# Optimization experiments

Hardware: AMD Instinct MI355X
Metric: run time of the kernel (lower is better)

## Reference

```python
import jax, jax.numpy as jnp
import numpy as np

NUM_AGENTS = 256
STATE_DIM = 12 * NUM_AGENTS
CONTROL_DIM = 4 * NUM_AGENTS
MASS = 0.5
HIDDEN = 100
BATCH = 8192


def lambertw(x):
    # Principal branch for x >= 0 via Halley iterations (jit/vjp friendly).
    w = jnp.log1p(x)
    for _ in range(30):
        ew = jnp.exp(w)
        f = w * ew - x
        denom = ew * (w + 1.0) - (w + 2.0) * f / (2.0 * (w + 1.0))
        w = w - f / denom
    return w


def setup_inputs() -> dict:
    key = jax.random.key(0)
    ks = jax.random.split(key, 8)
    scale1 = 1.0 / np.sqrt(STATE_DIM + 1)
    scale2 = 1.0 / np.sqrt(HIDDEN)
    return {
        "z": jax.random.normal(ks[0], (BATCH, STATE_DIM), dtype=jnp.float32),
        "t": jax.random.uniform(ks[1], (BATCH, 1), dtype=jnp.float32),
        "W1": jax.random.normal(ks[2], (STATE_DIM + 1, HIDDEN), dtype=jnp.float32) * scale1,
        "b1": jnp.zeros((HIDDEN,), dtype=jnp.float32),
        "W2": jax.random.normal(ks[3], (HIDDEN, HIDDEN), dtype=jnp.float32) * scale2,
        "b2": jnp.zeros((HIDDEN,), dtype=jnp.float32),
        "W3": jax.random.normal(ks[4], (HIDDEN, STATE_DIM), dtype=jnp.float32) * scale2,
        "b3": jnp.zeros((STATE_DIM,), dtype=jnp.float32),
    }


def reference(z, t, W1, b1, W2, b2, W3, b3):
    # p_net: MLP on (t, z) producing cost parameters p (B, STATE_DIM)
    x = jnp.concatenate([t, z], axis=-1)
    h = jnp.tanh(x @ W1 + b1)
    h = jnp.tanh(h @ W2 + b2)
    p = h @ W3 + b3

    B = p.shape[0]
    pr = p.reshape(B, NUM_AGENTS, 12)
    # Linear cost vector c over controls: agent components (x,y,z adjoints)/m, psi, theta, phi.
    c = jnp.stack(
        [(pr[..., 6] + pr[..., 7] + pr[..., 8]) / MASS, pr[..., 9], pr[..., 10], pr[..., 11]],
        axis=-1,
    ).reshape(B, CONTROL_DIM)

    # Closed-form solution of min_u c^T u + exp(alpha * ||u||^2), alpha = 0.5/N:
    # u* = -k c with 2*alpha*k*exp(alpha*k^2*s) = 1, s = ||c||^2
    # => k = sqrt(W(s/(2*alpha)) / (2*alpha*s))
    alpha = 0.5 / NUM_AGENTS
    s = jnp.sum(c * c, axis=-1)  # (B,)
    w = lambertw(s / (2.0 * alpha))
    safe_s = jnp.where(s > 0, s, 1.0)
    k = jnp.sqrt(w / (2.0 * alpha * safe_s))
    k = jnp.where(s > 0, k, 0.0)
    ustar = -k[:, None] * c  # (B, CONTROL_DIM)
    return ustar
```

## Files before the change

### kernel.cpp

```cpp
#include <hip/hip_runtime.h>

#define DEV __device__ __forceinline__

typedef __bf16 bf16x8 __attribute__((ext_vector_type(8)));
typedef float f32x4 __attribute__((ext_vector_type(4)));
typedef short s16x8 __attribute__((ext_vector_type(8)));
typedef unsigned short u16x8 __attribute__((ext_vector_type(8)));

constexpr int B_ = 8192;
constexpr int S_ = 3072;
constexpr int H_ = 100;
constexpr int NP_ = 128;
constexpr int C_ = 1024;
constexpr int KS_ = 64;
constexpr int NSPLIT_ = 8;
constexpr int KSP_ = S_ / NSPLIT_;
constexpr int NIT_ = KSP_ / KS_;
constexpr int MT_ = 64;

constexpr size_t OFF_W1b = 0;
constexpr size_t OFF_W2b = OFF_W1b + (size_t)NP_ * S_ * 2;
constexpr size_t OFF_W3c = OFF_W2b + (size_t)NP_ * NP_ * 2;
constexpr size_t OFF_b3c = OFF_W3c + (size_t)C_ * NP_ * 2;
constexpr size_t OFF_part = OFF_b3c + (size_t)C_ * 4;

DEV unsigned short f2bf(float f) {
  union { float f; unsigned u; } x; x.f = f;
  return (unsigned short)((x.u + 0x7FFFu + ((x.u >> 16) & 1u)) >> 16);
}

DEV float lambertw0(float x) {
  float w = log1pf(x);
#pragma unroll
  for (int i = 0; i < 10; ++i) {
    float ew = expf(w);
    float f = fmaf(w, ew, -x);
    float wp1 = w + 1.0f;
    float den = ew * wp1 - (w + 2.0f) * f / (2.0f * wp1);
    w = w - f / den;
  }
  return w;
}

DEV void gload16(const void* g, void* l) {
  __builtin_amdgcn_global_load_lds((const __attribute__((address_space(1))) unsigned int*)g,
                                   (__attribute__((address_space(3))) unsigned int*)l, 16, 0, 0);
}

__global__ void k0_prep(const float* __restrict__ W1, const float* __restrict__ W2,
                        const float* __restrict__ W3, const float* __restrict__ b3,
                        unsigned char* __restrict__ ws) {
  int idx = blockIdx.x * 256 + threadIdx.x;
  constexpr int R1 = NP_ * S_;
  constexpr int R2 = R1 + NP_ * NP_;
  constexpr int R3 = R2 + C_ * NP_;
  constexpr int R4 = R3 + C_;
  if (idx < R1) {
    int n = idx / S_, k = idx - n * S_;
    float v = (n < H_) ? W1[(size_t)(k + 1) * H_ + n] : 0.0f;
    ((unsigned short*)(ws + OFF_W1b))[idx] = f2bf(v);
  } else if (idx < R2) {
    int j = idx - R1;
    int n = j >> 7, k = j & 127;
    float v = (n < H_ && k < H_) ? W2[(size_t)k * H_ + n] : 0.0f;
    ((unsigned short*)(ws + OFF_W2b))[j] = f2bf(v);
  } else if (idx < R3) {
    int j = idx - R2;
    int n = j >> 7, k = j & 127;
    float v = 0.0f;
    if (k < H_) {
      int a = n >> 2, cmp = n & 3;
      const float* row = W3 + (size_t)k * S_ + a * 12;
      v = (cmp == 0) ? 2.0f * (row[6] + row[7] + row[8]) : row[8 + cmp];
    }
    ((unsigned short*)(ws + OFF_W3c))[j] = f2bf(v);
  } else if (idx < R4) {
    int n = idx - R3;
    int a = n >> 2, cmp = n & 3;
    const float* row = b3 + a * 12;
    float v = (cmp == 0) ? 2.0f * (row[6] + row[7] + row[8]) : row[8 + cmp];
    ((float*)(ws + OFF_b3c))[n] = v;
  }
}

__global__ __launch_bounds__(256, 4) void k1_gemm1(
    const float* __restrict__ z, const unsigned char* __restrict__ wsr,
    float* __restrict__ part) {
  __shared__ __align__(16) unsigned char ldsB[2][16384];

  const int tid = threadIdx.x;
  const int lane = tid & 63;
  const int w = tid >> 6;
  const int bid = blockIdx.x;
  const int rt = bid >> 3;
  const int h = bid & 7;
  const int rowbase = rt * MT_;
  const int k0 = h * KSP_;

  const unsigned short* W1b = (const unsigned short*)(wsr + OFF_W1b);

  const int arow = rowbase + w * 16 + (lane & 15);
  const int o8 = (lane >> 4) * 8;
  const float* zrp = z + (size_t)arow * S_ + k0 + o8;

  const int w4 = w * 4;
  const unsigned short* bsrc = W1b + (size_t)(w4 * 8 + (lane >> 3)) * S_ + k0
                               + (((lane & 7) ^ (lane >> 3)) * 8);

  const int kb0 = (lane >> 4) * 16;

  f32x4 acc[8];
#pragma unroll
  for (int e = 0; e < 8; ++e) acc[e] = f32x4{0.f, 0.f, 0.f, 0.f};

#define GLOAD_B(buf, kof) do {                                               \
    _Pragma("unroll")                                                        \
    for (int s = 0; s < 4; ++s)                                              \
      gload16(bsrc + (size_t)s * 8 * S_ + (kof),                             \
              ldsB[buf] + (w4 + s) * 1024);                                  \
  } while (0)

#define ISSUE_A(F0A, F0B, F1A, F1B, kof) do {                                \
    (F0A) = *(const float4*)(zrp + (kof));                                   \
    (F0B) = *(const float4*)(zrp + (kof) + 4);                               \
    (F1A) = *(const float4*)(zrp + (kof) + 32);                              \
    (F1B) = *(const float4*)(zrp + (kof) + 36);                              \
  } while (0)

#define COMPUTE(F0A, F0B, F1A, F1B, buf) do {                                \
    union { u16x8 u; bf16x8 b; } a0c, a1c;                                   \
    a0c.u[0] = f2bf((F0A).x); a0c.u[1] = f2bf((F0A).y);                      \
    a0c.u[2] = f2bf((F0A).z); a0c.u[3] = f2bf((F0A).w);                      \
    a0c.u[4] = f2bf((F0B).x); a0c.u[5] = f2bf((F0B).y);                      \
    a0c.u[6] = f2bf((F0B).z); a0c.u[7] = f2bf((F0B).w);                      \
    a1c.u[0] = f2bf((F1A).x); a1c.u[1] = f2bf((F1A).y);                      \
    a1c.u[2] = f2bf((F1A).z); a1c.u[3] = f2bf((F1A).w);                      \
    a1c.u[4] = f2bf((F1B).x); a1c.u[5] = f2bf((F1B).y);                      \
    a1c.u[6] = f2bf((F1B).z); a1c.u[7] = f2bf((F1B).w);                      \
    _Pragma("unroll")                                                        \
    for (int e = 0; e < 8; ++e) {                                            \
      int n = e * 16 + (lane & 15);                                          \
      bf16x8 bb0 = *(const bf16x8*)(ldsB[buf] + ((n * 128 + 0 + kb0) ^ ((n & 7) << 4)));  \
      bf16x8 bb1 = *(const bf16x8*)(ldsB[buf] + ((n * 128 + 64 + kb0) ^ ((n & 7) << 4))); \
      acc[e] = __builtin_amdgcn_mfma_f32_16x16x32_bf16(a0c.b, bb0, acc[e], 0, 0, 0);      \
      acc[e] = __builtin_amdgcn_mfma_f32_16x16x32_bf16(a1c.b, bb1, acc[e], 0, 0, 0);      \
    }                                                                        \
  } while (0)

  float4 e0a, e0b, e1a, e1b;
  float4 o0a, o0b, o1a, o1b;

  GLOAD_B(0, 0);
  ISSUE_A(e0a, e0b, e1a, e1b, 0);
  __syncthreads();

  for (int tt = 0; tt < NIT_; tt += 2) {
    {
      const bool more = (tt + 1 < NIT_);
      if (more) {
        GLOAD_B(1, (size_t)(tt + 1) * KS_);
        ISSUE_A(o0a, o0b, o1a, o1b, (tt + 1) * KS_);
      }
      COMPUTE(e0a, e0b, e1a, e1b, 0);
      __syncthreads();
    }
    {
      const bool more = (tt + 2 < NIT_);
      if (more) {
        GLOAD_B(0, (size_t)(tt + 2) * KS_);
        ISSUE_A(e0a, e0b, e1a, e1b, (tt + 2) * KS_);
      }
      COMPUTE(o0a, o0b, o1a, o1b, 1);
      __syncthreads();
    }
  }
#undef GLOAD_B
#undef ISSUE_A
#undef COMPUTE

  float* pout = part + (size_t)h * B_ * NP_;
#pragma unroll
  for (int e = 0; e < 8; ++e) {
    int col = e * 16 + (lane & 15);
#pragma unroll
    for (int i = 0; i < 4; ++i) {
      int r = w * 16 + ((lane >> 4) << 2) + i;
      pout[(size_t)(rowbase + r) * NP_ + col] = acc[e][i];
    }
  }
}

__global__ __launch_bounds__(512, 2) void k2_fused(
    const float* __restrict__ part, const float* __restrict__ t,
    const float* __restrict__ W1, const float* __restrict__ b1,
    const float* __restrict__ b2, const unsigned char* __restrict__ wsr,
    float* __restrict__ uo) {
  __shared__ __align__(16) unsigned char ldsA[8192];
  __shared__ __align__(16) unsigned char ldsB[2][32768];
  __shared__ float s_part[32][4];
  __shared__ float k_lds[32];

  const int tid = threadIdx.x;
  const int lane = tid & 63;
  const int w = tid >> 6;
  const int m = w & 1;
  const int q = w >> 1;
  const int rowbase = blockIdx.x * 32;

  const unsigned short* W2b = (const unsigned short*)(wsr + OFF_W2b);
  const unsigned short* W3cb = (const unsigned short*)(wsr + OFF_W3c);
  const float* b3c = (const float*)(wsr + OFF_b3c);

  {
    const int row = tid >> 4;
    const int col0 = (tid & 15) * 8;
    const float* p0 = part + (size_t)(rowbase + row) * NP_ + col0;
    f32x4 v[2];
#pragma unroll
    for (int p = 0; p < 2; ++p) {
      v[p] = *(const f32x4*)(p0 + p * 4);
#pragma unroll
      for (int hh = 1; hh < NSPLIT_; ++hh) {
        f32x4 u2 = *(const f32x4*)(p0 + (size_t)hh * B_ * NP_ + p * 4);
        v[p][0] += u2[0]; v[p][1] += u2[1]; v[p][2] += u2[2]; v[p][3] += u2[3];
      }
    }
    const float tv = t[rowbase + row];
    u16x8 o;
#pragma unroll
    for (int j = 0; j < 8; ++j) {
      int col = col0 + j;
      float b1c = (col < H_) ? b1[col] : 0.0f;
      float w1t = (col < H_) ? W1[col] : 0.0f;
      float pre = v[j >> 2][j & 3] + b1c + tv * w1t;
      o[j] = f2bf(tanhf(pre));
    }
    *(u16x8*)(ldsA + ((row * 256 + col0 * 2) ^ ((row & 7) << 4))) = o;
  }
#pragma unroll
  for (int s = 0; s < 4; ++s) {
    int p = s * 512 + tid;
    int n = p >> 4, k16 = p & 15;
    s16x8 v2 = *(const s16x8*)(W2b + n * 128 + k16 * 8);
    *(s16x8*)(ldsB[1] + ((n * 256 + k16 * 16) ^ ((n & 7) << 4))) = v2;
    s16x8 v3 = *(const s16x8*)(W3cb + (size_t)n * NP_ + k16 * 8);
    *(s16x8*)(ldsB[0] + ((n * 256 + k16 * 16) ^ ((n & 7) << 4))) = v3;
  }
  if (tid < 128) s_part[tid >> 2][tid & 3] = 0.0f;
  __syncthreads();

  const int r0 = m * 16 + (lane & 15);
  const int kb0 = (lane >> 4) * 16;

  f32x4 acc2[2];
  acc2[0] = f32x4{0.f, 0.f, 0.f, 0.f};
  acc2[1] = f32x4{0.f, 0.f, 0.f, 0.f};
#pragma unroll
  for (int ks = 0; ks < 4; ++ks) {
    bf16x8 a = *(const bf16x8*)(ldsA + ((r0 * 256 + ks * 64 + kb0) ^ ((r0 & 7) << 4)));
#pragma unroll
    for (int e = 0; e < 2; ++e) {
      int n = (q * 2 + e) * 16 + (lane & 15);
      bf16x8 b = *(const bf16x8*)(ldsB[1] + ((n * 256 + ks * 64 + kb0) ^ ((n & 7) << 4)));
      acc2[e] = __builtin_amdgcn_mfma_f32_16x16x32_bf16(a, b, acc2[e], 0, 0, 0);
    }
  }
  __syncthreads();
#pragma unroll
  for (int e = 0; e < 2; ++e) {
    int col = (q * 2 + e) * 16 + (lane & 15);
    float b2c = (col < H_) ? b2[col] : 0.0f;
#pragma unroll
    for (int i = 0; i < 4; ++i) {
      int r = m * 16 + ((lane >> 4) << 2) + i;
      float hh = tanhf(acc2[e][i] + b2c);
      *(unsigned short*)(ldsA + ((r * 256 + col * 2) ^ ((r & 7) << 4))) = f2bf(hh);
    }
  }
  __syncthreads();

  bf16x8 af[4];
#pragma unroll
  for (int ks = 0; ks < 4; ++ks)
    af[ks] = *(const bf16x8*)(ldsA + ((r0 * 256 + ks * 64 + kb0) ^ ((r0 & 7) << 4)));

  f32x4 fr[16];
#pragma unroll
  for (int i = 0; i < 16; ++i) fr[i] = f32x4{0.f, 0.f, 0.f, 0.f};

#pragma unroll 8
  for (int ch = 0; ch < 8; ++ch) {
    const int cur = ch & 1;
    const bool more = ch < 7;
    s16x8 st0, st1, st2, st3;
    if (more) {
      int base = (ch + 1) * 128;
      { int p = tid;            int n = p >> 4, k16 = p & 15; st0 = *(const s16x8*)(W3cb + (size_t)(base + n) * NP_ + k16 * 8); }
      { int p = 512 + tid;      int n = p >> 4, k16 = p & 15; st1 = *(const s16x8*)(W3cb + (size_t)(base + n) * NP_ + k16 * 8); }
      { int p = 1024 + tid;     int n = p >> 4, k16 = p & 15; st2 = *(const s16x8*)(W3cb + (size_t)(base + n) * NP_ + k16 * 8); }
      { int p = 1536 + tid;     int n = p >> 4, k16 = p & 15; st3 = *(const s16x8*)(W3cb + (size_t)(base + n) * NP_ + k16 * 8); }
    }
#pragma unroll
    for (int e = 0; e < 2; ++e) {
      int nloc = (q + 4 * e) * 16 + (lane & 15);
#pragma unroll
      for (int ks = 0; ks < 4; ++ks) {
        bf16x8 b = *(const bf16x8*)(ldsB[cur] + ((nloc * 256 + ks * 64 + kb0) ^ ((nloc & 7) << 4)));
        fr[ch * 2 + e] = __builtin_amdgcn_mfma_f32_16x16x32_bf16(af[ks], b, fr[ch * 2 + e], 0, 0, 0);
      }
    }
    if (more) {
      unsigned char* Bn = ldsB[cur ^ 1];
      { int p = tid;        int n = p >> 4, k16 = p & 15; *(s16x8*)(Bn + ((n * 256 + k16 * 16) ^ ((n & 7) << 4))) = st0; }
      { int p = 512 + tid;  int n = p >> 4, k16 = p & 15; *(s16x8*)(Bn + ((n * 256 + k16 * 16) ^ ((n & 7) << 4))) = st1; }
      { int p = 1024 + tid; int n = p >> 4, k16 = p & 15; *(s16x8*)(Bn + ((n * 256 + k16 * 16) ^ ((n & 7) << 4))) = st2; }
      { int p = 1536 + tid; int n = p >> 4, k16 = p & 15; *(s16x8*)(Bn + ((n * 256 + k16 * 16) ^ ((n & 7) << 4))) = st3; }
    }
    __syncthreads();
  }

#pragma unroll
  for (int fi = 0; fi < 16; ++fi) {
    int ch = fi >> 1, e = fi & 1;
    int col = (ch * 8 + q + 4 * e) * 16 + (lane & 15);
    float bc = b3c[col];
    fr[fi][0] += bc; fr[fi][1] += bc; fr[fi][2] += bc; fr[fi][3] += bc;
  }
#pragma unroll
  for (int i = 0; i < 4; ++i) {
    float v = 0.f;
#pragma unroll
    for (int fi = 0; fi < 16; ++fi) v += fr[fi][i] * fr[fi][i];
    v += __shfl_xor(v, 1);
    v += __shfl_xor(v, 2);
    v += __shfl_xor(v, 4);
    v += __shfl_xor(v, 8);
    if ((lane & 15) == 0) s_part[m * 16 + ((lane >> 4) << 2) + i][q] = v;
  }
  __syncthreads();
  if (tid < 32) {
    float s = s_part[tid][0] + s_part[tid][1] + s_part[tid][2] + s_part[tid][3];
    float kk = 0.0f;
    if (s > 0.0f) {
      float wv = lambertw0(s * 256.0f);
      kk = sqrtf(wv * 256.0f / s);
    }
    k_lds[tid] = kk;
  }
  __syncthreads();
#pragma unroll
  for (int fi = 0; fi < 16; ++fi) {
    int ch = fi >> 1, e = fi & 1;
    int col = (ch * 8 + q + 4 * e) * 16 + (lane & 15);
#pragma unroll
    for (int i = 0; i < 4; ++i) {
      int r = m * 16 + ((lane >> 4) << 2) + i;
      uo[(size_t)(rowbase + r) * C_ + col] = -k_lds[r] * fr[fi][i];
    }
  }
}

extern "C" void kernel_launch(void* const* d_in, const int* in_sizes, int n_in,
                              void* d_out, int out_size, void* d_ws, size_t ws_size,
                              hipStream_t stream) {
  const float* z  = (const float*)d_in[0];
  const float* t  = (const float*)d_in[1];
  const float* W1 = (const float*)d_in[2];
  const float* b1 = (const float*)d_in[3];
  const float* W2 = (const float*)d_in[4];
  const float* b2 = (const float*)d_in[5];
  const float* W3 = (const float*)d_in[6];
  const float* b3 = (const float*)d_in[7];
  float* out = (float*)d_out;
  unsigned char* ws = (unsigned char*)d_ws;
  float* part = (float*)(ws + OFF_part);

  constexpr int PREP_ELEMS = NP_ * S_ + NP_ * NP_ + C_ * NP_ + C_;
  k0_prep<<<(PREP_ELEMS + 255) / 256, 256, 0, stream>>>(W1, W2, W3, b3, ws);
  k1_gemm1<<<(B_ / MT_) * NSPLIT_, 256, 0, stream>>>(z, ws, part);
  k2_fused<<<B_ / 32, 512, 0, stream>>>(part, t, W1, b1, b2, ws, out);
}
```

Measured before the change: 56.66 us.

## Stage full W1 k-slice in LDS once and preload z rows into registers

The first GEMM kernel now copies its entire bf16 W1 k-slice (128x384) into swizzled LDS once per block, then processes 256 rows per block with 512 threads. Each wave loads its whole z strip into registers up front and runs the MFMA loop without per-step barriers or double buffering. This removes repeated W1 reloads and synchronisation, at the cost of heavy LDS use (96KB), high register pressure, fewer blocks in the grid and less load/compute overlap.

```diff
diff --git a/kernel.cpp b/kernel.cpp
--- a/kernel.cpp
+++ b/kernel.cpp
@@ -12,11 +12,9 @@
 constexpr int H_ = 100;
 constexpr int NP_ = 128;
 constexpr int C_ = 1024;
-constexpr int KS_ = 64;
 constexpr int NSPLIT_ = 8;
 constexpr int KSP_ = S_ / NSPLIT_;
-constexpr int NIT_ = KSP_ / KS_;
-constexpr int MT_ = 64;
+constexpr int MROW_ = 256;
 
 constexpr size_t OFF_W1b = 0;
 constexpr size_t OFF_W2b = OFF_W1b + (size_t)NP_ * S_ * 2;
@@ -40,11 +38,6 @@
     w = w - f / den;
   }
   return w;
-}
-
-DEV void gload16(const void* g, void* l) {
-  __builtin_amdgcn_global_load_lds((const __attribute__((address_space(1))) unsigned int*)g,
-                                   (__attribute__((address_space(3))) unsigned int*)l, 16, 0, 0);
 }
 
 __global__ void k0_prep(const float* __restrict__ W1, const float* __restrict__ W2,
@@ -83,109 +76,79 @@
   }
 }
 
-__global__ __launch_bounds__(256, 4) void k1_gemm1(
+__global__ __launch_bounds__(512, 2) void k1_gemm1(
     const float* __restrict__ z, const unsigned char* __restrict__ wsr,
     float* __restrict__ part) {
-  __shared__ __align__(16) unsigned char ldsB[2][16384];
+  __shared__ __align__(16) unsigned char ldsB[128 * 768];
 
   const int tid = threadIdx.x;
   const int lane = tid & 63;
   const int w = tid >> 6;
   const int bid = blockIdx.x;
-  const int rt = bid >> 3;
   const int h = bid & 7;
-  const int rowbase = rt * MT_;
+  const int rowblk = bid >> 3;
+  const int rowbase = rowblk * MROW_;
   const int k0 = h * KSP_;
 
   const unsigned short* W1b = (const unsigned short*)(wsr + OFF_W1b);
 
-  const int arow = rowbase + w * 16 + (lane & 15);
-  const int o8 = (lane >> 4) * 8;
-  const float* zrp = z + (size_t)arow * S_ + k0 + o8;
-
-  const int w4 = w * 4;
-  const unsigned short* bsrc = W1b + (size_t)(w4 * 8 + (lane >> 3)) * S_ + k0
-                               + (((lane & 7) ^ (lane >> 3)) * 8);
-
-  const int kb0 = (lane >> 4) * 16;
-
-  f32x4 acc[8];
-#pragma unroll
-  for (int e = 0; e < 8; ++e) acc[e] = f32x4{0.f, 0.f, 0.f, 0.f};
-
-#define GLOAD_B(buf, kof) do {                                               \
-    _Pragma("unroll")                                                        \
-    for (int s = 0; s < 4; ++s)                                              \
-      gload16(bsrc + (size_t)s * 8 * S_ + (kof),                             \
-              ldsB[buf] + (w4 + s) * 1024);                                  \
-  } while (0)
-
-#define ISSUE_A(F0A, F0B, F1A, F1B, kof) do {                                \
-    (F0A) = *(const float4*)(zrp + (kof));                                   \
-    (F0B) = *(const float4*)(zrp + (kof) + 4);                               \
-    (F1A) = *(const float4*)(zrp + (kof) + 32);                              \
-    (F1B) = *(const float4*)(zrp + (kof) + 36);                              \
-  } while (0)
-
-#define COMPUTE(F0A, F0B, F1A, F1B, buf) do {                                \
-    union { u16x8 u; bf16x8 b; } a0c, a1c;                                   \
-    a0c.u[0] = f2bf((F0A).x); a0c.u[1] = f2bf((F0A).y);                      \
-    a0c.u[2] = f2bf((F0A).z); a0c.u[3] = f2bf((F0A).w);                      \
-    a0c.u[4] = f2bf((F0B).x); a0c.u[5] = f2bf((F0B).y);                      \
-    a0c.u[6] = f2bf((F0B).z); a0c.u[7] = f2bf((F0B).w);                      \
-    a1c.u[0] = f2bf((F1A).x); a1c.u[1] = f2bf((F1A).y);                      \
-    a1c.u[2] = f2bf((F1A).z); a1c.u[3] = f2bf((F1A).w);                      \
-    a1c.u[4] = f2bf((F1B).x); a1c.u[5] = f2bf((F1B).y);                      \
-    a1c.u[6] = f2bf((F1B).z); a1c.u[7] = f2bf((F1B).w);                      \
-    _Pragma("unroll")                                                        \
-    for (int e = 0; e < 8; ++e) {                                            \
-      int n = e * 16 + (lane & 15);                                          \
-      bf16x8 bb0 = *(const bf16x8*)(ldsB[buf] + ((n * 128 + 0 + kb0) ^ ((n & 7) << 4)));  \
-      bf16x8 bb1 = *(const bf16x8*)(ldsB[buf] + ((n * 128 + 64 + kb0) ^ ((n & 7) << 4))); \
-      acc[e] = __builtin_amdgcn_mfma_f32_16x16x32_bf16(a0c.b, bb0, acc[e], 0, 0, 0);      \
-      acc[e] = __builtin_amdgcn_mfma_f32_16x16x32_bf16(a1c.b, bb1, acc[e], 0, 0, 0);      \
-    }                                                                        \
-  } while (0)
-
-  float4 e0a, e0b, e1a, e1b;
-  float4 o0a, o0b, o1a, o1b;
-
-  GLOAD_B(0, 0);
-  ISSUE_A(e0a, e0b, e1a, e1b, 0);
-  __syncthreads();
-
-  for (int tt = 0; tt < NIT_; tt += 2) {
-    {
-      const bool more = (tt + 1 < NIT_);
-      if (more) {
-        GLOAD_B(1, (size_t)(tt + 1) * KS_);
-        ISSUE_A(o0a, o0b, o1a, o1b, (tt + 1) * KS_);
+#pragma unroll
+  for (int i = 0; i < 12; ++i) {
+    int j = i * 512 + tid;
+    int n = j / 48, c = j - n * 48;
+    s16x8 v = *(const s16x8*)(W1b + (size_t)n * S_ + k0 + c * 8);
+    int pc = (c & ~7) | ((c & 7) ^ (n & 7));
+    *(s16x8*)(ldsB + n * 768 + pc * 16) = v;
+  }
+  __syncthreads();
+
+  const int rl = lane & 15;
+  const int o4 = lane >> 4;
+
+  float* pout = part + (size_t)h * B_ * NP_;
+
+#pragma unroll
+  for (int g2 = 0; g2 < 2; ++g2) {
+    const int grp = w * 2 + g2;
+    const int arow = rowbase + grp * 16 + rl;
+    const float* zp = z + (size_t)arow * S_ + k0 + o4 * 8;
+
+    float4 zr0[12], zr1[12];
+#pragma unroll
+    for (int ks = 0; ks < 12; ++ks) {
+      zr0[ks] = *(const float4*)(zp + ks * 32);
+      zr1[ks] = *(const float4*)(zp + ks * 32 + 4);
+    }
+
+    f32x4 acc[8];
+#pragma unroll
+    for (int e = 0; e < 8; ++e) acc[e] = f32x4{0.f, 0.f, 0.f, 0.f};
+
+#pragma unroll
+    for (int ks = 0; ks < 12; ++ks) {
+      union { u16x8 u; bf16x8 b; } af;
+      af.u[0] = f2bf(zr0[ks].x); af.u[1] = f2bf(zr0[ks].y);
+      af.u[2] = f2bf(zr0[ks].z); af.u[3] = f2bf(zr0[ks].w);
+      af.u[4] = f2bf(zr1[ks].x); af.u[5] = f2bf(zr1[ks].y);
+      af.u[6] = f2bf(zr1[ks].z); af.u[7] = f2bf(zr1[ks].w);
+#pragma unroll
+      for (int e = 0; e < 8; ++e) {
+        int n = e * 16 + rl;
+        int c = ks * 4 + o4;
+        int pc = (c & ~7) | ((c & 7) ^ (n & 7));
+        bf16x8 bb = *(const bf16x8*)(ldsB + n * 768 + pc * 16);
+        acc[e] = __builtin_amdgcn_mfma_f32_16x16x32_bf16(af.b, bb, acc[e], 0, 0, 0);
       }
-      COMPUTE(e0a, e0b, e1a, e1b, 0);
-      __syncthreads();
-    }
-    {
-      const bool more = (tt + 2 < NIT_);
-      if (more) {
-        GLOAD_B(0, (size_t)(tt + 2) * KS_);
-        ISSUE_A(e0a, e0b, e1a, e1b, (tt + 2) * KS_);
+    }
+
+#pragma unroll
+    for (int e = 0; e < 8; ++e) {
+      int col = e * 16 + rl;
+#pragma unroll
+      for (int i = 0; i < 4; ++i) {
+        int r = rowbase + grp * 16 + o4 * 4 + i;
+        pout[(size_t)r * NP_ + col] = acc[e][i];
       }
-      COMPUTE(o0a, o0b, o1a, o1b, 1);
-      __syncthreads();
-    }
-  }
-#undef GLOAD_B
-#undef ISSUE_A
-#undef COMPUTE
-
-  float* pout = part + (size_t)h * B_ * NP_;
-#pragma unroll
-  for (int e = 0; e < 8; ++e) {
-    int col = e * 16 + (lane & 15);
-#pragma unroll
-    for (int i = 0; i < 4; ++i) {
-      int r = w * 16 + ((lane >> 4) << 2) + i;
-      pout[(size_t)(rowbase + r) * NP_ + col] = acc[e][i];
     }
   }
 }
@@ -377,6 +340,6 @@
 
   constexpr int PREP_ELEMS = NP_ * S_ + NP_ * NP_ + C_ * NP_ + C_;
   k0_prep<<<(PREP_ELEMS + 255) / 256, 256, 0, stream>>>(W1, W2, W3, b3, ws);
-  k1_gemm1<<<(B_ / MT_) * NSPLIT_, 256, 0, stream>>>(z, ws, part);
+  k1_gemm1<<<(B_ / MROW_) * NSPLIT_, 512, 0, stream>>>(z, ws, part);
   k2_fused<<<B_ / 32, 512, 0, stream>>>(part, t, W1, b1, b2, ws, out);
 }
```

Measured after the change: 55.35 us. 2.3% less time.
